# Kernel tuning notes

Hardware: AMD Instinct MI355X
Metric: run time of the kernel (lower is better)

Reference implementation:

```python
import jax, jax.numpy as jnp
import numpy as np

N = 50000      # n_nodes
E = 800000     # edges (before self-loops)
IN = 128       # in_dim
HID = 32       # hidden_dim (per-head out channels)
HEADS = 4
EMB = 128      # embed_dim
LAYERS = 3
NEG_SLOPE = 0.2  # PyG GATv2 default leaky_relu slope


def _layer_norm(x, g, b):
    mu = jnp.mean(x, axis=-1, keepdims=True)
    var = jnp.var(x, axis=-1, keepdims=True)
    return g * (x - mu) / jnp.sqrt(var + 1e-5) + b


def _gatv2(h, src, dst, n, Wl, bl, Wr, br, att, bias):
    # GATv2Conv (PyG semantics, share_weights=False, concat=True).
    H, C = att.shape
    xl = (h @ Wl + bl).reshape(n, H, C)   # target (i) transform
    xr = (h @ Wr + br).reshape(n, H, C)   # source (j) transform
    x_i = xl[dst]                          # [Etot, H, C] gather
    x_j = xr[src]
    e = jax.nn.leaky_relu(x_i + x_j, NEG_SLOPE)
    logit = jnp.einsum('ehc,hc->eh', e, att)          # [Etot, H]
    # segment softmax over destination node (every node has a self-loop)
    m = jax.ops.segment_max(logit, dst, num_segments=n)
    ex = jnp.exp(logit - m[dst])
    den = jax.ops.segment_sum(ex, dst, num_segments=n)
    alpha = ex / (den[dst] + 1e-16)
    out = jax.ops.segment_sum(alpha[..., None] * x_j, dst, num_segments=n)
    return out.reshape(n, H * C) + bias


def setup_inputs() -> dict:
    key = jax.random.key(0)
    ks = iter(jax.random.split(key, 64))
    d = {}
    d['x'] = jax.random.normal(next(ks), (N, IN), jnp.float32)
    d['edge_index'] = jax.random.randint(next(ks), (2, E), 0, N, dtype=jnp.int64)

    def w(shape, fan):
        return jax.random.normal(next(ks), shape, jnp.float32) / np.float32(np.sqrt(fan))

    HC = HID * HEADS
    d['W_in'] = w((IN, HID), IN); d['b_in'] = jnp.zeros((HID,), jnp.float32)
    for i in range(LAYERS):
        ic = HID if i == 0 else HC
        d[f'Wl{i}'] = w((ic, HC), ic); d[f'bl{i}'] = jnp.zeros((HC,), jnp.float32)
        d[f'Wr{i}'] = w((ic, HC), ic); d[f'br{i}'] = jnp.zeros((HC,), jnp.float32)
        d[f'att{i}'] = w((HEADS, HID), HID)
        d[f'bo{i}'] = jnp.zeros((HC,), jnp.float32)
        d[f'g{i}'] = jnp.ones((HC,), jnp.float32)
        d[f'be{i}'] = jnp.zeros((HC,), jnp.float32)
    d['W_out'] = w((HC, EMB), HC); d['b_out'] = jnp.zeros((EMB,), jnp.float32)
    return d


def reference(x, edge_index, W_in, b_in,
              Wl0, bl0, Wr0, br0, att0, bo0, g0, be0,
              Wl1, bl1, Wr1, br1, att1, bo1, g1, be1,
              Wl2, bl2, Wr2, br2, att2, bo2, g2, be2,
              W_out, b_out):
    n = x.shape[0]
    loops = jnp.arange(n, dtype=edge_index.dtype)  # add_self_loops=True
    src = jnp.concatenate([edge_index[0], loops])
    dst = jnp.concatenate([edge_index[1], loops])

    h = jax.nn.gelu(x @ W_in + b_in, approximate=False)
    layers = [(Wl0, bl0, Wr0, br0, att0, bo0, g0, be0),
              (Wl1, bl1, Wr1, br1, att1, bo1, g1, be1),
              (Wl2, bl2, Wr2, br2, att2, bo2, g2, be2)]
    for (Wl, bl, Wr, br, att, bo, g, be) in layers:
        h_new = jax.nn.gelu(_layer_norm(_gatv2(h, src, dst, n, Wl, bl, Wr, br, att, bo), g, be), approximate=False)
        h = h + h_new if h.shape == h_new.shape else h_new  # dropout = identity (eval)
    out = h @ W_out + b_out
    norm = jnp.maximum(jnp.linalg.norm(out, axis=-1, keepdims=True), 1e-12)
    return out / norm
```

## Files before the change

kernel.cpp:

```cpp
#include <hip/hip_runtime.h>
#include <hip/hip_bf16.h>
#include <math.h>

#define N_NODES 50000
#define N_EDGES 800000
#define IN_DIM  128
#define HC_DIM  128
#define HID_C   32
#define SCAN_NB 196
#define LOG2E   1.4426950408889634f

typedef __attribute__((ext_vector_type(8))) short short8;
typedef __attribute__((ext_vector_type(4))) short short4v;
typedef __attribute__((ext_vector_type(4))) float f32x4;
typedef _Float16 hf8 __attribute__((ext_vector_type(8)));
typedef _Float16 hf2 __attribute__((ext_vector_type(2)));
typedef unsigned int uint4v __attribute__((ext_vector_type(4)));

__device__ __forceinline__ float gelu_f(float x){
    return 0.5f*x*(1.0f + erff(x*0.7071067811865475f));
}

__device__ __forceinline__ void split2(float f, short& h, short& l){
    __hip_bfloat16 bh = __float2bfloat16(f);
    float r = f - __bfloat162float(bh);
    __hip_bfloat16 blo = __float2bfloat16(r);
    h = *reinterpret_cast<short*>(&bh);
    l = *reinterpret_cast<short*>(&blo);
}
__device__ __forceinline__ unsigned short f2h(float f){
    _Float16 h = (_Float16)f;
    return __builtin_bit_cast(unsigned short, h);
}
__device__ __forceinline__ float bf2f(unsigned short u){
    return __uint_as_float(((unsigned)u)<<16);
}

__global__ __launch_bounds__(256) void k_count(const int* __restrict__ dst, int* __restrict__ cnt,
                                               int* __restrict__ rank){
    int b = blockIdx.x*1024 + threadIdx.x;
    #pragma unroll
    for(int i=0;i<4;i++){
        int e = b + i*256;
        if(e < N_EDGES) rank[e] = atomicAdd(&cnt[dst[e]], 1);
    }
}

__global__ __launch_bounds__(256) void k_scan1(const int* __restrict__ cnt, int* __restrict__ rowptr,
                                               int* __restrict__ part){
    __shared__ int sh[256];
    int t=threadIdx.x; int i=blockIdx.x*256+t;
    int v = (i<N_NODES)? cnt[i] : 0;
    sh[t]=v; __syncthreads();
    for(int off=1; off<256; off<<=1){
        int y = (t>=off)? sh[t-off] : 0;
        __syncthreads();
        sh[t] += y;
        __syncthreads();
    }
    if(i<N_NODES) rowptr[i] = sh[t]-v;
    if(t==255) part[blockIdx.x] = sh[255];
}

__global__ __launch_bounds__(256) void k_scan2(int* __restrict__ part){
    __shared__ int sh[256];
    int t=threadIdx.x;
    int v = (t<SCAN_NB)? part[t] : 0;
    sh[t]=v; __syncthreads();
    for(int off=1; off<256; off<<=1){
        int y=(t>=off)? sh[t-off]:0;
        __syncthreads();
        sh[t]+=y;
        __syncthreads();
    }
    if(t<SCAN_NB) part[t] = sh[t]-v;
}

__global__ __launch_bounds__(256) void k_scan3(int* __restrict__ rowptr, const int* __restrict__ part){
    int t=threadIdx.x; int i=blockIdx.x*256+t;
    if(i<N_NODES) rowptr[i] += part[blockIdx.x];
    if(i==0) rowptr[N_NODES]=N_EDGES;
}

__global__ __launch_bounds__(256) void k_fill(const int* __restrict__ src, const int* __restrict__ dst,
                                              const int* __restrict__ rowptr, const int* __restrict__ rank,
                                              int* __restrict__ col){
    int b = blockIdx.x*1024 + threadIdx.x;
    #pragma unroll
    for(int i=0;i<4;i++){
        int e = b + i*256;
        if(e < N_EDGES) col[rowptr[dst[e]] + rank[e]] = src[e];
    }
}

__global__ __launch_bounds__(256) void k_splitW(const float* __restrict__ W0, const float* __restrict__ W1,
                                                const float* __restrict__ W2, const float* __restrict__ W3,
                                                const float* __restrict__ W4, const float* __restrict__ W5,
                                                const float* __restrict__ W6, short* __restrict__ WT){
    int bx = blockIdx.x;
    int m, kc;
    if(bx < 2){ m = bx; kc = 0; }
    else { m = 2 + (bx-2)/4; kc = (bx-2)&3; }
    const float* src; int K; size_t off;
    switch(m){
        case 0: src=W0; K=32;  off=0;      break;
        case 1: src=W1; K=32;  off=8192;   break;
        case 2: src=W2; K=128; off=16384;  break;
        case 3: src=W3; K=128; off=49152;  break;
        case 4: src=W4; K=128; off=81920;  break;
        case 5: src=W5; K=128; off=114688; break;
        default:src=W6; K=128; off=147456; break;
    }
    short* hi = WT + off;
    short* lo = hi + (size_t)K*HC_DIM;
    #pragma unroll
    for(int i=0;i<16;i++){
        int idx = threadIdx.x + i*256;
        int k = kc*32 + (idx>>7);
        int n = idx & 127;
        float f = src[(size_t)k*HC_DIM + n];
        short h,l; split2(f,h,l);
        hi[(size_t)n*K + k] = h;
        lo[(size_t)n*K + k] = l;
    }
}

__global__ __launch_bounds__(256) void k_gemm_in(const float* __restrict__ x, const float* __restrict__ W,
                                                 const float* __restrict__ b,
                                                 short* __restrict__ hhi, short* __restrict__ hlo){
    int id = blockIdx.x*256+threadIdx.x;
    int r = id>>5, c = id&31;
    const float4* x4 = (const float4*)(x + (size_t)r*IN_DIM);
    float acc=0.f;
    #pragma unroll 8
    for(int k=0;k<IN_DIM/4;k++){
        float4 xv = x4[k];
        acc = fmaf(xv.x, W[(4*k  )*HID_C+c], acc);
        acc = fmaf(xv.y, W[(4*k+1)*HID_C+c], acc);
        acc = fmaf(xv.z, W[(4*k+2)*HID_C+c], acc);
        acc = fmaf(xv.w, W[(4*k+3)*HID_C+c], acc);
    }
    float v = gelu_f(acc + b[c]);
    short hh,ll; split2(v,hh,ll);
    hhi[(size_t)r*HID_C+c] = hh;
    hlo[(size_t)r*HID_C+c] = ll;
}

template<int K, bool PAIR, bool NORM>
__global__ __launch_bounds__(256) void k_mfma(const short* __restrict__ Ahi, const short* __restrict__ Alo,
                                              const short* __restrict__ WTl, const float* __restrict__ bl,
                                              const short* __restrict__ WTr, const float* __restrict__ br,
                                              float* __restrict__ XLf, unsigned short* __restrict__ XLh,
                                              unsigned short* __restrict__ XR16){
    constexpr int LDS_K = 40;
    constexpr int NCH = K / 32;
    __shared__ short As_hi[64*LDS_K], As_lo[64*LDS_K];
    __shared__ short Bh0[128*LDS_K], Bl0[128*LDS_K];
    __shared__ short Bh1[PAIR?128*LDS_K:1], Bl1[PAIR?128*LDS_K:1];
    __shared__ float ssq[NORM?256:1];

    int t = threadIdx.x;
    int lane = t & 63, wave = t >> 6;
    int quad = lane >> 4, ml = lane & 15;
    int rbase = blockIdx.x * 64;

    const short* WTl_lo = WTl + (size_t)K*HC_DIM;
    const short* WTr_lo = PAIR ? (WTr + (size_t)K*HC_DIM) : nullptr;

    f32x4 accL[4][2], accR[4][2];
    #pragma unroll
    for(int i=0;i<4;i++)
        #pragma unroll
        for(int j=0;j<2;j++){ accL[i][j]=(f32x4){0,0,0,0}; accR[i][j]=(f32x4){0,0,0,0}; }

    int r = t >> 2, seg = t & 3;
    int gr = rbase + r; if(gr >= N_NODES) gr = N_NODES-1;

    for(int c=0; c<NCH; c++){
        if(c) __syncthreads();
        size_t ka = (size_t)gr*K + c*32 + seg*8;
        *(short8*)(As_hi + r*LDS_K + seg*8) = *(const short8*)(Ahi + ka);
        *(short8*)(As_lo + r*LDS_K + seg*8) = *(const short8*)(Alo + ka);
        #pragma unroll
        for(int u=0; u<2; u++){
            int uu = t + u*256;
            int n = uu >> 2, sg = uu & 3;
            size_t kw = (size_t)n*K + c*32 + sg*8;
            *(short8*)(Bh0 + n*LDS_K + sg*8) = *(const short8*)(WTl + kw);
            *(short8*)(Bl0 + n*LDS_K + sg*8) = *(const short8*)(WTl_lo + kw);
            if(PAIR){
                *(short8*)(Bh1 + n*LDS_K + sg*8) = *(const short8*)(WTr + kw);
                *(short8*)(Bl1 + n*LDS_K + sg*8) = *(const short8*)(WTr_lo + kw);
            }
        }
        __syncthreads();

        int k0 = quad*8;
        short8 ah[4], al[4];
        #pragma unroll
        for(int i=0;i<4;i++){
            ah[i] = *(const short8*)(As_hi + (16*i + ml)*LDS_K + k0);
            al[i] = *(const short8*)(As_lo + (16*i + ml)*LDS_K + k0);
        }
        #pragma unroll
        for(int j=0;j<2;j++){
            int nrow = j*64 + wave*16 + ml;
            short8 bh = *(const short8*)(Bh0 + nrow*LDS_K + k0);
            short8 blo = *(const short8*)(Bl0 + nrow*LDS_K + k0);
            #pragma unroll
            for(int i=0;i<4;i++){
                accL[i][j] = __builtin_amdgcn_mfma_f32_16x16x32_bf16(ah[i], bh,  accL[i][j], 0,0,0);
                accL[i][j] = __builtin_amdgcn_mfma_f32_16x16x32_bf16(ah[i], blo, accL[i][j], 0,0,0);
                accL[i][j] = __builtin_amdgcn_mfma_f32_16x16x32_bf16(al[i], bh,  accL[i][j], 0,0,0);
            }
            if(PAIR){
                short8 ch = *(const short8*)(Bh1 + nrow*LDS_K + k0);
                short8 cl = *(const short8*)(Bl1 + nrow*LDS_K + k0);
                #pragma unroll
                for(int i=0;i<4;i++){
                    accR[i][j] = __builtin_amdgcn_mfma_f32_16x16x32_bf16(ah[i], ch, accR[i][j], 0,0,0);
                    accR[i][j] = __builtin_amdgcn_mfma_f32_16x16x32_bf16(ah[i], cl, accR[i][j], 0,0,0);
                    accR[i][j] = __builtin_amdgcn_mfma_f32_16x16x32_bf16(al[i], ch, accR[i][j], 0,0,0);
                }
            }
        }
    }

    int col0 = wave*16 + ml, col1 = 64 + wave*16 + ml;
    float bL0 = bl[col0], bL1 = bl[col1];

    if(NORM){
        #pragma unroll
        for(int i=0;i<4;i++){
            #pragma unroll
            for(int rr=0;rr<4;rr++){
                float v0 = accL[i][0][rr] + bL0;
                float v1 = accL[i][1][rr] + bL1;
                float p = v0*v0 + v1*v1;
                p += __shfl_xor(p,1); p += __shfl_xor(p,2);
                p += __shfl_xor(p,4); p += __shfl_xor(p,8);
                if(ml==0) ssq[wave*64 + 16*i + quad*4 + rr] = p;
            }
        }
        __syncthreads();
        #pragma unroll
        for(int i=0;i<4;i++){
            #pragma unroll
            for(int rr=0;rr<4;rr++){
                int row = 16*i + quad*4 + rr;
                int grr = rbase + row;
                if(grr < N_NODES){
                    float tot = ssq[row] + ssq[64+row] + ssq[128+row] + ssq[192+row];
                    float inv = 1.0f / fmaxf(sqrtf(tot), 1e-12f);
                    XLf[(size_t)grr*HC_DIM + col0] = (accL[i][0][rr] + bL0) * inv;
                    XLf[(size_t)grr*HC_DIM + col1] = (accL[i][1][rr] + bL1) * inv;
                }
            }
        }
    } else {
        float bR0 = PAIR ? br[col0] : 0.f, bR1 = PAIR ? br[col1] : 0.f;
        #pragma unroll
        for(int i=0;i<4;i++){
            #pragma unroll
            for(int rr=0;rr<4;rr++){
                int grr = rbase + 16*i + quad*4 + rr;
                if(grr < N_NODES){
                    XLh[(size_t)grr*HC_DIM + col0] = f2h(accL[i][0][rr] + bL0);
                    XLh[(size_t)grr*HC_DIM + col1] = f2h(accL[i][1][rr] + bL1);
                    if(PAIR){
                        XR16[(size_t)grr*HC_DIM + col0] = f2h(accR[i][0][rr] + bR0);
                        XR16[(size_t)grr*HC_DIM + col1] = f2h(accR[i][1][rr] + bR1);
                    }
                }
            }
        }
    }
}

__global__ __launch_bounds__(256) void k_node(const unsigned short* __restrict__ XLH, const unsigned short* __restrict__ XR,
    const int* __restrict__ rowptr, const int* __restrict__ colidx,
    const float* __restrict__ att, const float* __restrict__ bo,
    const float* __restrict__ gg, const float* __restrict__ be,
    const short* __restrict__ hold_hi, const short* __restrict__ hold_lo,
    short* __restrict__ hi_out, short* __restrict__ lo_out)
{
    int wave=threadIdx.x>>6, lane=threadIdx.x&63;
    int node = blockIdx.x*4+wave;
    int qd = lane >> 4, cl = lane & 15;
    int c8 = cl << 3;
    int ch2 = c8 + (qd<<1);

    #define H2(v,k) __builtin_shufflevector(v, v, 2*(k), 2*(k)+1)
    #define LOADH(j, xv) { xv = *(const hf8*)((const _Float16*)XR + ((size_t)((unsigned)(j)<<7)) + c8); }
#if defined(__has_builtin) && __has_builtin(__builtin_amdgcn_fdot2)
    #define LOGIT(xv, q) { \
        hf8 u_ = xlh + xv; \
        hf8 a_ = __builtin_bit_cast(hf8, __builtin_bit_cast(uint4v, u_) & 0x7fff7fffu); \
        float qa_ = __builtin_amdgcn_fdot2(H2(u_,0), H2(av6,0), 0.f, false); \
        float qb_ = __builtin_amdgcn_fdot2(H2(a_,0), H2(av4,0), 0.f, false); \
        qa_ = __builtin_amdgcn_fdot2(H2(u_,1), H2(av6,1), qa_, false); \
        qb_ = __builtin_amdgcn_fdot2(H2(a_,1), H2(av4,1), qb_, false); \
        qa_ = __builtin_amdgcn_fdot2(H2(u_,2), H2(av6,2), qa_, false); \
        qb_ = __builtin_amdgcn_fdot2(H2(a_,2), H2(av4,2), qb_, false); \
        qa_ = __builtin_amdgcn_fdot2(H2(u_,3), H2(av6,3), qa_, false); \
        qb_ = __builtin_amdgcn_fdot2(H2(a_,3), H2(av4,3), qb_, false); \
        q = qa_ + qb_; \
        q += __shfl_xor(q,1); q += __shfl_xor(q,2); }
#else
    #define LOGIT(xv, q) { \
        hf8 u_ = xlh + xv; \
        hf8 a_ = __builtin_bit_cast(hf8, __builtin_bit_cast(uint4v, u_) & 0x7fff7fffu); \
        q = 0.f; \
        _Pragma("unroll") \
        for(int k_=0;k_<8;k_++) q = fmaf((float)u_[k_], (float)av6[k_], fmaf((float)a_[k_], (float)av4[k_], q)); \
        q += __shfl_xor(q,1); q += __shfl_xor(q,2); }
#endif

    int beg = rowptr[node], end = rowptr[node+1];
    hf8 xlh = *(const hf8*)((const _Float16*)XLH + ((size_t)((unsigned)node<<7)) + c8);
    hf8 xs; LOADH(node, xs)
    float hres0 = 0.f, hres1 = 0.f;
    if(hold_hi){
        short2 hh = *(const short2*)(hold_hi + (size_t)node*HC_DIM + ch2);
        short2 hl = *(const short2*)(hold_lo + (size_t)node*HC_DIM + ch2);
        hres0 = bf2f((unsigned short)hh.x) + bf2f((unsigned short)hl.x);
        hres1 = bf2f((unsigned short)hh.y) + bf2f((unsigned short)hl.y);
    }

    float4 aa = *(const float4*)(att + c8);
    float4 abv = *(const float4*)(att + c8 + 4);
    float af[8] = {aa.x,aa.y,aa.z,aa.w,abv.x,abv.y,abv.z,abv.w};
    hf8 av6, av4;
    const float s6 = 0.6f*LOG2E, s4 = 0.4f*LOG2E;
    #pragma unroll
    for(int k=0;k<8;k++){
        av6[k] = (_Float16)(af[k]*s6);
        av4[k] = (_Float16)(af[k]*s4);
    }

    float qs; LOGIT(xs, qs)
    float m, ls, acc[8];
    int deg = end - beg;

    if(deg < 32){
        hf8 xv[8]; float q[8];
        if(deg > 0){
            int last = end - 1;
            int qb = beg + (qd<<2);
            #pragma unroll
            for(int t=0;t<8;t++){
                int ii = qb + ((t>>2)<<4) + (t&3);
                int a = (ii <= last) ? ii : last;
                int j = colidx[a];
                LOADH(j, xv[t])
            }
            #pragma unroll
            for(int t=0;t<8;t++){
                float qq; LOGIT(xv[t], qq)
                int ii = qb + ((t>>2)<<4) + (t&3);
                q[t] = (ii <= last) ? qq : -INFINITY;
            }
        } else {
            hf8 z;
            #pragma unroll
            for(int k=0;k<8;k++) z[k] = (_Float16)0.f;
            #pragma unroll
            for(int t=0;t<8;t++){ xv[t] = z; q[t] = -INFINITY; }
        }
        float nm = (qd==0) ? qs : -1e30f;
        #pragma unroll
        for(int t=0;t<8;t++) nm = fmaxf(nm, q[t]);
        float es = (qd==0) ? exp2f(qs-nm) : 0.f;
        ls = es;
        #pragma unroll
        for(int k=0;k<8;k++) acc[k] = es*(float)xs[k];
        #pragma unroll
        for(int t=0;t<8;t++){
            float e = exp2f(q[t]-nm);
            ls += e;
            #pragma unroll
            for(int k=0;k<8;k++) acc[k] = fmaf(e, (float)xv[t][k], acc[k]);
        }
        m = nm;
    } else {
        #define UPDATE4 { \
            float nm = fmaxf(m, fmaxf(fmaxf(q0,q1),fmaxf(q2,q3))); \
            float sc = exp2f(m-nm); \
            float e0=exp2f(q0-nm), e1=exp2f(q1-nm), e2=exp2f(q2-nm), e3=exp2f(q3-nm); \
            ls = fmaf(ls, sc, (e0+e1)+(e2+e3)); \
            _Pragma("unroll") \
            for(int k=0;k<8;k++) \
                acc[k] = fmaf(acc[k], sc, fmaf(e0,(float)x0[k], fmaf(e1,(float)x1[k], fmaf(e2,(float)x2[k], e3*(float)x3[k])))); \
            m = nm; }

        if(qd==0){
            m = qs; ls = 1.f;
            #pragma unroll
            for(int k=0;k<8;k++) acc[k] = (float)xs[k];
        } else {
            m = -1e30f; ls = 0.f;
            #pragma unroll
            for(int k=0;k<8;k++) acc[k] = 0.f;
        }
        int nb = deg >> 4;
        int base = beg;
        int qoff = qd << 2;
        for(int b=0; b<nb; b++, base += 16){
            int b2 = base + qoff;
            int j0 = colidx[b2], j1 = colidx[b2+1], j2 = colidx[b2+2], j3 = colidx[b2+3];
            hf8 x0,x1,x2,x3;
            LOADH(j0,x0) LOADH(j1,x1) LOADH(j2,x2) LOADH(j3,x3)
            float q0,q1,q2,q3;
            LOGIT(x0,q0) LOGIT(x1,q1) LOGIT(x2,q2) LOGIT(x3,q3)
            UPDATE4
        }
        if(base < end){
            int b2 = base + qoff;
            int j0 = (b2  <end)? colidx[b2]   : node;
            int j1 = (b2+1<end)? colidx[b2+1] : node;
            int j2 = (b2+2<end)? colidx[b2+2] : node;
            int j3 = (b2+3<end)? colidx[b2+3] : node;
            hf8 x0,x1,x2,x3;
            LOADH(j0,x0) LOADH(j1,x1) LOADH(j2,x2) LOADH(j3,x3)
            float q0,q1,q2,q3;
            LOGIT(x0,q0) LOGIT(x1,q1) LOGIT(x2,q2) LOGIT(x3,q3)
            if(b2+1>=end) q1 = -INFINITY;
            if(b2+2>=end) q2 = -INFINITY;
            if(b2+3>=end) q3 = -INFINITY;
            if(b2 < end){
                UPDATE4
            }
        }
        #undef UPDATE4
    }
    #undef LOGIT
    #undef LOADH
    #undef H2

    #pragma unroll
    for(int mk=16; mk<=32; mk<<=1){
        float mo  = __shfl_xor(m, mk);
        float lso = __shfl_xor(ls, mk);
        float ao[8];
        #pragma unroll
        for(int k=0;k<8;k++) ao[k] = __shfl_xor(acc[k], mk);
        float nm = fmaxf(m, mo);
        float s0 = exp2f(m-nm), s1 = exp2f(mo-nm);
        ls = ls*s0 + lso*s1;
        #pragma unroll
        for(int k=0;k<8;k++) acc[k] = acc[k]*s0 + ao[k]*s1;
        m = nm;
    }

    float inv = 1.0f/ls;
    float4 b0 = *(const float4*)(bo + c8);
    float4 b1 = *(const float4*)(bo + c8 + 4);
    float bof[8] = {b0.x,b0.y,b0.z,b0.w,b1.x,b1.y,b1.z,b1.w};
    float o[8];
    #pragma unroll
    for(int k=0;k<8;k++) o[k] = fmaf(acc[k], inv, bof[k]);
    float s1v = ((o[0]+o[1])+(o[2]+o[3])) + ((o[4]+o[5])+(o[6]+o[7]));
    float s2v = o[0]*o[0];
    #pragma unroll
    for(int k=1;k<8;k++) s2v = fmaf(o[k],o[k],s2v);
    #pragma unroll
    for(int mk=1;mk<16;mk<<=1){ s1v += __shfl_xor(s1v,mk); s2v += __shfl_xor(s2v,mk); }
    float mean = s1v*(1.f/128.f);
    float var  = s2v*(1.f/128.f) - mean*mean;
    float rstd = rsqrtf(var + 1e-5f);

    float oa = (qd&2) ? ((qd&1)? o[6] : o[4]) : ((qd&1)? o[2] : o[0]);
    float ob = (qd&2) ? ((qd&1)? o[7] : o[5]) : ((qd&1)? o[3] : o[1]);
    float2 g2  = *(const float2*)(gg + ch2);
    float2 be2 = *(const float2*)(be + ch2);
    float r0 = gelu_f(fmaf(g2.x*(oa-mean), rstd, be2.x)) + hres0;
    float r1 = gelu_f(fmaf(g2.y*(ob-mean), rstd, be2.y)) + hres1;
    short h0,l0,h1,l1;
    split2(r0,h0,l0); split2(r1,h1,l1);
    *(short2*)(hi_out + (size_t)node*HC_DIM + ch2) = make_short2(h0,h1);
    *(short2*)(lo_out + (size_t)node*HC_DIM + ch2) = make_short2(l0,l1);
}

extern "C" void kernel_launch(void* const* d_in, const int* in_sizes, int n_in,
                              void* d_out, int out_size, void* d_ws, size_t ws_size,
                              hipStream_t stream)
{
    const float* x   = (const float*)d_in[0];
    const int*   ei  = (const int*)  d_in[1];
    const float* Win = (const float*)d_in[2];
    const float* bin = (const float*)d_in[3];
    const float *Wl[3], *bl[3], *Wr[3], *br[3], *att[3], *bo[3], *gg[3], *be[3];
    for(int i=0;i<3;i++){
        const int base = 4 + 8*i;
        Wl[i]=(const float*)d_in[base+0]; bl[i]=(const float*)d_in[base+1];
        Wr[i]=(const float*)d_in[base+2]; br[i]=(const float*)d_in[base+3];
        att[i]=(const float*)d_in[base+4]; bo[i]=(const float*)d_in[base+5];
        gg[i]=(const float*)d_in[base+6]; be[i]=(const float*)d_in[base+7];
    }
    const float* Wout=(const float*)d_in[28];
    const float* bout=(const float*)d_in[29];
    float* out = (float*)d_out;

    char* w = (char*)d_ws;
    unsigned short* XLH = (unsigned short*)w; w += (size_t)N_NODES*HC_DIM*2;
    unsigned short* XR16 = (unsigned short*)w; w += (size_t)N_NODES*HC_DIM*2;
    short* hAhi = (short*)w; w += (size_t)N_NODES*HC_DIM*2;
    short* hAlo = (short*)w; w += (size_t)N_NODES*HC_DIM*2;
    short* hBhi = (short*)w; w += (size_t)N_NODES*HC_DIM*2;
    short* hBlo = (short*)w; w += (size_t)N_NODES*HC_DIM*2;
    short* WT   = (short*)w; w += (size_t)180224*2;
    int* rowptr = (int*)w;  w += (size_t)(N_NODES+2)*4;
    int* cursor = (int*)w;  w += (size_t)N_NODES*4;
    int* colidx = (int*)w;  w += (size_t)N_EDGES*4;
    int* rank   = (int*)w;  w += (size_t)N_EDGES*4;
    int* part   = (int*)w;  w += 256*4;

    const int* srcp = ei;
    const int* dstp = ei + N_EDGES;

    const short* WTl0 = WT + 0;      const short* WTr0 = WT + 8192;
    const short* WTl1 = WT + 16384;  const short* WTr1 = WT + 49152;
    const short* WTl2 = WT + 81920;  const short* WTr2 = WT + 114688;
    const short* WTo  = WT + 147456;

    k_splitW<<<22,256,0,stream>>>(Wl[0],Wr[0],Wl[1],Wr[1],Wl[2],Wr[2],Wout, WT);
    hipMemsetAsync(cursor, 0, (size_t)N_NODES*4, stream);
    k_count <<<782,256, 0, stream>>>(dstp, cursor, rank);
    k_scan1 <<<SCAN_NB,256,0,stream>>>(cursor, rowptr, part);
    k_scan2 <<<1,   256, 0, stream>>>(part);
    k_scan3 <<<SCAN_NB,256,0,stream>>>(rowptr, part);
    k_fill  <<<782,256, 0, stream>>>(srcp, dstp, rowptr, rank, colidx);
    k_gemm_in<<<6250,256,0,stream>>>(x, Win, bin, hAhi, hAlo);

    k_mfma<32,true,false><<<782,256,0,stream>>>(hAhi, hAlo, WTl0, bl[0], WTr0, br[0],
                                                nullptr, XLH, XR16);
    k_node<<<12500,256,0,stream>>>(XLH,XR16,rowptr,colidx,att[0],bo[0],gg[0],be[0],
                                   (const short*)nullptr, (const short*)nullptr, hBhi, hBlo);

    k_mfma<128,true,false><<<782,256,0,stream>>>(hBhi, hBlo, WTl1, bl[1], WTr1, br[1],
                                                 nullptr, XLH, XR16);
    k_node<<<12500,256,0,stream>>>(XLH,XR16,rowptr,colidx,att[1],bo[1],gg[1],be[1],
                                   hBhi, hBlo, hAhi, hAlo);

    k_mfma<128,true,false><<<782,256,0,stream>>>(hAhi, hAlo, WTl2, bl[2], WTr2, br[2],
                                                 nullptr, XLH, XR16);
    k_node<<<12500,256,0,stream>>>(XLH,XR16,rowptr,colidx,att[2],bo[2],gg[2],be[2],
                                   hAhi, hAlo, hBhi, hBlo);

    k_mfma<128,false,true><<<782,256,0,stream>>>(hBhi, hBlo, WTo, bout, nullptr, nullptr,
                                                 out, nullptr, nullptr);
}
```

Measured before the change: 509.2 us.

## Drop LDS staging in MFMA GEMM and remove low-degree fast path in node kernel

The split-bf16 GEMM kernel no longer stages A and W tiles through shared memory with barriers. Each wave now loads its MFMA fragments straight from global memory, relying on L1/L2 for reuse of the small weight matrices. The node aggregation kernel drops its special path for degree below 32 and always uses the 16-edge-chunk online-softmax loop. This trades duplicated global or cache loads and less latency hiding for fewer syncs, less LDS use, and simpler code.

New measurement: 543.8 us. 1.07x slower.

```diff
diff --git a/kernel.cpp b/kernel.cpp
--- a/kernel.cpp
+++ b/kernel.cpp
@@ -11,10 +11,8 @@
 #define LOG2E   1.4426950408889634f
 
 typedef __attribute__((ext_vector_type(8))) short short8;
-typedef __attribute__((ext_vector_type(4))) short short4v;
 typedef __attribute__((ext_vector_type(4))) float f32x4;
 typedef _Float16 hf8 __attribute__((ext_vector_type(8)));
-typedef _Float16 hf2 __attribute__((ext_vector_type(2)));
 typedef unsigned int uint4v __attribute__((ext_vector_type(4)));
 
 __device__ __forceinline__ float gelu_f(float x){
@@ -147,18 +145,12 @@
 }
 
 template<int K, bool PAIR, bool NORM>
-__global__ __launch_bounds__(256) void k_mfma(const short* __restrict__ Ahi, const short* __restrict__ Alo,
-                                              const short* __restrict__ WTl, const float* __restrict__ bl,
-                                              const short* __restrict__ WTr, const float* __restrict__ br,
-                                              float* __restrict__ XLf, unsigned short* __restrict__ XLh,
-                                              unsigned short* __restrict__ XR16){
-    constexpr int LDS_K = 40;
-    constexpr int NCH = K / 32;
-    __shared__ short As_hi[64*LDS_K], As_lo[64*LDS_K];
-    __shared__ short Bh0[128*LDS_K], Bl0[128*LDS_K];
-    __shared__ short Bh1[PAIR?128*LDS_K:1], Bl1[PAIR?128*LDS_K:1];
+__global__ __launch_bounds__(256) void k_mm(const short* __restrict__ Ahi, const short* __restrict__ Alo,
+                                            const short* __restrict__ WTl, const float* __restrict__ bl,
+                                            const short* __restrict__ WTr, const float* __restrict__ br,
+                                            float* __restrict__ XLf, unsigned short* __restrict__ XLh,
+                                            unsigned short* __restrict__ XR16){
     __shared__ float ssq[NORM?256:1];
-
     int t = threadIdx.x;
     int lane = t & 63, wave = t >> 6;
     int quad = lane >> 4, ml = lane & 15;
@@ -173,40 +165,27 @@
         #pragma unroll
         for(int j=0;j<2;j++){ accL[i][j]=(f32x4){0,0,0,0}; accR[i][j]=(f32x4){0,0,0,0}; }
 
-    int r = t >> 2, seg = t & 3;
-    int gr = rbase + r; if(gr >= N_NODES) gr = N_NODES-1;
-
-    for(int c=0; c<NCH; c++){
-        if(c) __syncthreads();
-        size_t ka = (size_t)gr*K + c*32 + seg*8;
-        *(short8*)(As_hi + r*LDS_K + seg*8) = *(const short8*)(Ahi + ka);
-        *(short8*)(As_lo + r*LDS_K + seg*8) = *(const short8*)(Alo + ka);
-        #pragma unroll
-        for(int u=0; u<2; u++){
-            int uu = t + u*256;
-            int n = uu >> 2, sg = uu & 3;
-            size_t kw = (size_t)n*K + c*32 + sg*8;
-            *(short8*)(Bh0 + n*LDS_K + sg*8) = *(const short8*)(WTl + kw);
-            *(short8*)(Bl0 + n*LDS_K + sg*8) = *(const short8*)(WTl_lo + kw);
-            if(PAIR){
-                *(short8*)(Bh1 + n*LDS_K + sg*8) = *(const short8*)(WTr + kw);
-                *(short8*)(Bl1 + n*LDS_K + sg*8) = *(const short8*)(WTr_lo + kw);
-            }
-        }
-        __syncthreads();
-
-        int k0 = quad*8;
+    int rowA[4];
+    #pragma unroll
+    for(int i=0;i<4;i++){
+        int rr = rbase + 16*i + ml;
+        rowA[i] = (rr < N_NODES) ? rr : (N_NODES-1);
+    }
+
+    #pragma unroll 2
+    for(int c=0; c<K/32; c++){
+        int k0 = c*32 + quad*8;
         short8 ah[4], al[4];
         #pragma unroll
         for(int i=0;i<4;i++){
-            ah[i] = *(const short8*)(As_hi + (16*i + ml)*LDS_K + k0);
-            al[i] = *(const short8*)(As_lo + (16*i + ml)*LDS_K + k0);
+            ah[i] = *(const short8*)(Ahi + (size_t)rowA[i]*K + k0);
+            al[i] = *(const short8*)(Alo + (size_t)rowA[i]*K + k0);
         }
         #pragma unroll
         for(int j=0;j<2;j++){
             int nrow = j*64 + wave*16 + ml;
-            short8 bh = *(const short8*)(Bh0 + nrow*LDS_K + k0);
-            short8 blo = *(const short8*)(Bl0 + nrow*LDS_K + k0);
+            short8 bh  = *(const short8*)(WTl    + (size_t)nrow*K + k0);
+            short8 blo = *(const short8*)(WTl_lo + (size_t)nrow*K + k0);
             #pragma unroll
             for(int i=0;i<4;i++){
                 accL[i][j] = __builtin_amdgcn_mfma_f32_16x16x32_bf16(ah[i], bh,  accL[i][j], 0,0,0);
@@ -214,8 +193,8 @@
                 accL[i][j] = __builtin_amdgcn_mfma_f32_16x16x32_bf16(al[i], bh,  accL[i][j], 0,0,0);
             }
             if(PAIR){
-                short8 ch = *(const short8*)(Bh1 + nrow*LDS_K + k0);
-                short8 cl = *(const short8*)(Bl1 + nrow*LDS_K + k0);
+                short8 ch = *(const short8*)(WTr    + (size_t)nrow*K + k0);
+                short8 cl = *(const short8*)(WTr_lo + (size_t)nrow*K + k0);
                 #pragma unroll
                 for(int i=0;i<4;i++){
                     accR[i][j] = __builtin_amdgcn_mfma_f32_16x16x32_bf16(ah[i], ch, accR[i][j], 0,0,0);
@@ -315,6 +294,15 @@
         for(int k_=0;k_<8;k_++) q = fmaf((float)u_[k_], (float)av6[k_], fmaf((float)a_[k_], (float)av4[k_], q)); \
         q += __shfl_xor(q,1); q += __shfl_xor(q,2); }
 #endif
+    #define UPDATE4 { \
+        float nm = fmaxf(m, fmaxf(fmaxf(q0,q1),fmaxf(q2,q3))); \
+        float sc = exp2f(m-nm); \
+        float e0=exp2f(q0-nm), e1=exp2f(q1-nm), e2=exp2f(q2-nm), e3=exp2f(q3-nm); \
+        ls = fmaf(ls, sc, (e0+e1)+(e2+e3)); \
+        _Pragma("unroll") \
+        for(int k=0;k<8;k++) \
+            acc[k] = fmaf(acc[k], sc, fmaf(e0,(float)x0[k], fmaf(e1,(float)x1[k], fmaf(e2,(float)x2[k], e3*(float)x3[k])))); \
+        m = nm; }
 
     int beg = rowptr[node], end = rowptr[node+1];
     hf8 xlh = *(const hf8*)((const _Float16*)XLH + ((size_t)((unsigned)node<<7)) + c8);
@@ -340,99 +328,47 @@
 
     float qs; LOGIT(xs, qs)
     float m, ls, acc[8];
-    int deg = end - beg;
-
-    if(deg < 32){
-        hf8 xv[8]; float q[8];
-        if(deg > 0){
-            int last = end - 1;
-            int qb = beg + (qd<<2);
-            #pragma unroll
-            for(int t=0;t<8;t++){
-                int ii = qb + ((t>>2)<<4) + (t&3);
-                int a = (ii <= last) ? ii : last;
-                int j = colidx[a];
-                LOADH(j, xv[t])
-            }
-            #pragma unroll
-            for(int t=0;t<8;t++){
-                float qq; LOGIT(xv[t], qq)
-                int ii = qb + ((t>>2)<<4) + (t&3);
-                q[t] = (ii <= last) ? qq : -INFINITY;
-            }
-        } else {
-            hf8 z;
-            #pragma unroll
-            for(int k=0;k<8;k++) z[k] = (_Float16)0.f;
-            #pragma unroll
-            for(int t=0;t<8;t++){ xv[t] = z; q[t] = -INFINITY; }
-        }
-        float nm = (qd==0) ? qs : -1e30f;
-        #pragma unroll
-        for(int t=0;t<8;t++) nm = fmaxf(nm, q[t]);
-        float es = (qd==0) ? exp2f(qs-nm) : 0.f;
-        ls = es;
-        #pragma unroll
-        for(int k=0;k<8;k++) acc[k] = es*(float)xs[k];
-        #pragma unroll
-        for(int t=0;t<8;t++){
-            float e = exp2f(q[t]-nm);
-            ls += e;
-            #pragma unroll
-            for(int k=0;k<8;k++) acc[k] = fmaf(e, (float)xv[t][k], acc[k]);
-        }
-        m = nm;
+    if(qd==0){
+        m = qs; ls = 1.f;
+        #pragma unroll
+        for(int k=0;k<8;k++) acc[k] = (float)xs[k];
     } else {
-        #define UPDATE4 { \
-            float nm = fmaxf(m, fmaxf(fmaxf(q0,q1),fmaxf(q2,q3))); \
-            float sc = exp2f(m-nm); \
-            float e0=exp2f(q0-nm), e1=exp2f(q1-nm), e2=exp2f(q2-nm), e3=exp2f(q3-nm); \
-            ls = fmaf(ls, sc, (e0+e1)+(e2+e3)); \
-            _Pragma("unroll") \
-            for(int k=0;k<8;k++) \
-                acc[k] = fmaf(acc[k], sc, fmaf(e0,(float)x0[k], fmaf(e1,(float)x1[k], fmaf(e2,(float)x2[k], e3*(float)x3[k])))); \
-            m = nm; }
-
-        if(qd==0){
-            m = qs; ls = 1.f;
-            #pragma unroll
-            for(int k=0;k<8;k++) acc[k] = (float)xs[k];
-        } else {
-            m = -1e30f; ls = 0.f;
-            #pragma unroll
-            for(int k=0;k<8;k++) acc[k] = 0.f;
-        }
-        int nb = deg >> 4;
-        int base = beg;
-        int qoff = qd << 2;
-        for(int b=0; b<nb; b++, base += 16){
-            int b2 = base + qoff;
-            int j0 = colidx[b2], j1 = colidx[b2+1], j2 = colidx[b2+2], j3 = colidx[b2+3];
-            hf8 x0,x1,x2,x3;
-            LOADH(j0,x0) LOADH(j1,x1) LOADH(j2,x2) LOADH(j3,x3)
-            float q0,q1,q2,q3;
-            LOGIT(x0,q0) LOGIT(x1,q1) LOGIT(x2,q2) LOGIT(x3,q3)
+        m = -1e30f; ls = 0.f;
+        #pragma unroll
+        for(int k=0;k<8;k++) acc[k] = 0.f;
+    }
+
+    int P = end - beg;
+    int nb = P >> 4;
+    int base = beg;
+    int qoff = qd << 2;
+    for(int b=0; b<nb; b++, base += 16){
+        int b2 = base + qoff;
+        int j0 = colidx[b2], j1 = colidx[b2+1], j2 = colidx[b2+2], j3 = colidx[b2+3];
+        hf8 x0,x1,x2,x3;
+        LOADH(j0,x0) LOADH(j1,x1) LOADH(j2,x2) LOADH(j3,x3)
+        float q0,q1,q2,q3;
+        LOGIT(x0,q0) LOGIT(x1,q1) LOGIT(x2,q2) LOGIT(x3,q3)
+        UPDATE4
+    }
+    if(base < end){
+        int b2 = base + qoff;
+        int j0 = (b2  <end)? colidx[b2]   : node;
+        int j1 = (b2+1<end)? colidx[b2+1] : node;
+        int j2 = (b2+2<end)? colidx[b2+2] : node;
+        int j3 = (b2+3<end)? colidx[b2+3] : node;
+        hf8 x0,x1,x2,x3;
+        LOADH(j0,x0) LOADH(j1,x1) LOADH(j2,x2) LOADH(j3,x3)
+        float q0,q1,q2,q3;
+        LOGIT(x0,q0) LOGIT(x1,q1) LOGIT(x2,q2) LOGIT(x3,q3)
+        if(b2+1>=end) q1 = -INFINITY;
+        if(b2+2>=end) q2 = -INFINITY;
+        if(b2+3>=end) q3 = -INFINITY;
+        if(b2 < end){
             UPDATE4
         }
-        if(base < end){
-            int b2 = base + qoff;
-            int j0 = (b2  <end)? colidx[b2]   : node;
-            int j1 = (b2+1<end)? colidx[b2+1] : node;
-            int j2 = (b2+2<end)? colidx[b2+2] : node;
-            int j3 = (b2+3<end)? colidx[b2+3] : node;
-            hf8 x0,x1,x2,x3;
-            LOADH(j0,x0) LOADH(j1,x1) LOADH(j2,x2) LOADH(j3,x3)
-            float q0,q1,q2,q3;
-            LOGIT(x0,q0) LOGIT(x1,q1) LOGIT(x2,q2) LOGIT(x3,q3)
-            if(b2+1>=end) q1 = -INFINITY;
-            if(b2+2>=end) q2 = -INFINITY;
-            if(b2+3>=end) q3 = -INFINITY;
-            if(b2 < end){
-                UPDATE4
-            }
-        }
-        #undef UPDATE4
-    }
+    }
+    #undef UPDATE4
     #undef LOGIT
     #undef LOADH
     #undef H2
@@ -532,21 +468,21 @@
     k_fill  <<<782,256, 0, stream>>>(srcp, dstp, rowptr, rank, colidx);
     k_gemm_in<<<6250,256,0,stream>>>(x, Win, bin, hAhi, hAlo);
 
-    k_mfma<32,true,false><<<782,256,0,stream>>>(hAhi, hAlo, WTl0, bl[0], WTr0, br[0],
-                                                nullptr, XLH, XR16);
+    k_mm<32,true,false><<<782,256,0,stream>>>(hAhi, hAlo, WTl0, bl[0], WTr0, br[0],
+                                              nullptr, XLH, XR16);
     k_node<<<12500,256,0,stream>>>(XLH,XR16,rowptr,colidx,att[0],bo[0],gg[0],be[0],
                                    (const short*)nullptr, (const short*)nullptr, hBhi, hBlo);
 
-    k_mfma<128,true,false><<<782,256,0,stream>>>(hBhi, hBlo, WTl1, bl[1], WTr1, br[1],
-                                                 nullptr, XLH, XR16);
+    k_mm<128,true,false><<<782,256,0,stream>>>(hBhi, hBlo, WTl1, bl[1], WTr1, br[1],
+                                               nullptr, XLH, XR16);
     k_node<<<12500,256,0,stream>>>(XLH,XR16,rowptr,colidx,att[1],bo[1],gg[1],be[1],
                                    hBhi, hBlo, hAhi, hAlo);
 
-    k_mfma<128,true,false><<<782,256,0,stream>>>(hAhi, hAlo, WTl2, bl[2], WTr2, br[2],
-                                                 nullptr, XLH, XR16);
+    k_mm<128,true,false><<<782,256,0,stream>>>(hAhi, hAlo, WTl2, bl[2], WTr2, br[2],
+                                               nullptr, XLH, XR16);
     k_node<<<12500,256,0,stream>>>(XLH,XR16,rowptr,colidx,att[2],bo[2],gg[2],be[2],
                                    hAhi, hAlo, hBhi, hBlo);
 
-    k_mfma<128,false,true><<<782,256,0,stream>>>(hBhi, hBlo, WTo, bout, nullptr, nullptr,
-                                                 out, nullptr, nullptr);
-}
+    k_mm<128,false,true><<<782,256,0,stream>>>(hBhi, hBlo, WTo, bout, nullptr, nullptr,
+                                               out, nullptr, nullptr);
+}
```
